# Kernel tuning notes

Hardware: AMD Instinct MI355X
Metric: run time of the kernel (lower is better)

The kernel has to match this reference:

```python
import jax, jax.numpy as jnp
import numpy as np

K = 100  # hard-coded in GWDLoss.forward


def _topk(scores, k=K):
    # CenterNet predict._topk: per-class topk then topk over classes.
    b, c, h, w = scores.shape
    topk_scores, topk_inds = jax.lax.top_k(scores.reshape(b, c, h * w), k)  # [b,c,k]
    topk_inds = topk_inds % (h * w)
    topk_ys = (topk_inds // w).astype(scores.dtype)
    topk_xs = (topk_inds % w).astype(scores.dtype)
    topk_score, topk_ind = jax.lax.top_k(topk_scores.reshape(b, c * k), k)  # [b,k]
    def g(t):
        return jnp.take_along_axis(t.reshape(b, c * k), topk_ind, axis=1)
    return topk_score, g(topk_inds), g(topk_xs), g(topk_ys)


def _transpose_and_gather_feat(feat, ind):
    b, c, h, w = feat.shape
    feat = feat.transpose(0, 2, 3, 1).reshape(b, h * w, c)  # [b,hw,c]
    idx = jnp.broadcast_to(ind[:, :, None], (b, ind.shape[1], c))
    return jnp.take_along_axis(feat, idx, axis=1)  # [b,K,c]


def xywhr2xyrs(xywhr):
    xywhr = xywhr.reshape(-1, 5)
    xy = xywhr[:, :2]
    wh = jnp.clip(xywhr[:, 2:4], 1e-7, 1e7)
    r = jnp.deg2rad(xywhr[:, 4])
    cos_r, sin_r = jnp.cos(r), jnp.sin(r)
    R = jnp.stack([cos_r, -sin_r, sin_r, cos_r], axis=-1).reshape(-1, 2, 2)
    S = 0.5 * wh[:, :, None] * jnp.eye(2, dtype=wh.dtype)  # diag_embed
    return xy, R, S


def gwd_loss(pred, target, tau=1.0, alpha=1.0):
    xy_p, R_p, S_p = xywhr2xyrs(pred)
    xy_t, R_t, S_t = xywhr2xyrs(target)
    xy_distance = jnp.sum((xy_p - xy_t) ** 2, axis=-1)
    Sigma_p = R_p @ (S_p ** 2) @ jnp.swapaxes(R_p, -1, -2)
    Sigma_t = R_t @ (S_t ** 2) @ jnp.swapaxes(R_t, -1, -2)
    dS_p = jnp.diagonal(S_p, axis1=-2, axis2=-1)
    dS_t = jnp.diagonal(S_t, axis1=-2, axis2=-1)
    whr = jnp.sum(dS_p ** 2, -1) + jnp.sum(dS_t ** 2, -1)
    _t = Sigma_p @ Sigma_t
    _t_tr = jnp.trace(_t, axis1=-2, axis2=-1)
    _t_det_sqrt = jnp.prod(dS_p, -1) * jnp.prod(dS_t, -1)
    whr = whr - 2.0 * jnp.sqrt(jnp.maximum(_t_tr + 2.0 * _t_det_sqrt, 0.0))
    distance = jnp.maximum(xy_distance + alpha * alpha * whr, 0.0)
    distance = jnp.log1p(distance)  # fun='log'
    return 1.0 - 1.0 / (tau + distance)  # tau=1.0 >= 1.0


def _forward(hm_p, ab_p, ang_p, hm_t, ab_t, ang_t, ind, reg_mask):
    mask = reg_mask.astype(jnp.float32)  # [B,K]
    pred_ab = _transpose_and_gather_feat(ab_p, ind)    # [B,K,2]
    pred_ang = _transpose_and_gather_feat(ang_p, ind)  # [B,K,1]
    mask_ab = mask[:, :, None]
    mask_ang = mask[:, :, None]
    _, _, xp, yp = _topk(hm_p)
    pred_xy = jnp.stack([xp, yp], axis=2)  # [B,K,2]
    pred = jnp.concatenate([pred_xy * mask_ab, pred_ab * 2.0 * mask_ab,
                            (pred_ang - 90.0) * mask_ang], axis=2)
    _, _, xt, yt = _topk(hm_t)
    target_xy = jnp.stack([xt, yt], axis=2)
    target = jnp.concatenate([target_xy * mask_ab, ab_t * 2.0 * mask_ab,
                              (ang_t - 90.0) * mask_ang], axis=2)
    return jnp.sum(gwd_loss(pred, target)) / (jnp.sum(mask) + 1e-8)


def setup_inputs() -> dict:
    key = jax.random.key(0)
    ks = jax.random.split(key, 8)
    B, H, W = 64, 256, 256
    return {
        "hm_p": jax.random.uniform(ks[0], (B, 1, H, W), jnp.float32),
        "ab_p": jax.random.uniform(ks[1], (B, 2, H, W), jnp.float32),
        "ang_p": jax.random.uniform(ks[2], (B, 1, H, W), jnp.float32),
        "hm_t": jax.random.uniform(ks[3], (B, 1, H, W), jnp.float32),
        "ab_t": jax.random.uniform(ks[4], (B, K, 2), jnp.float32),
        "ang_t": jax.random.uniform(ks[5], (B, K, 1), jnp.float32),
        "ind": jax.random.randint(ks[6], (B, K), 0, H * W, jnp.int32),
        "reg_mask": jax.random.randint(ks[7], (B, K), 0, 2, jnp.int32),
    }


def reference(hm_p, ab_p, ang_p, hm_t, ab_t, ang_t, ind, reg_mask):
    return _forward(hm_p, ab_p, ang_p, hm_t, ab_t, ang_t, ind, reg_mask)
```

## Files before the change

kernel.cpp:

```cpp
#include <hip/hip_runtime.h>
#include <stdint.h>

#define HW 65536
#define WIMG 256
#define TOPK 100
#define CAP2 2048
#define CAPC 64
#define NCHUNK 8
#define NGROUP 128
#define FTHR 512

__device__ __forceinline__ uint32_t fkey(float v) {
    uint32_t b = __float_as_uint(v);
    return b ^ ((b & 0x80000000u) ? 0xFFFFFFFFu : 0x80000000u);
}

#define CAND_OFF  0
#define CNT_OFF   524288
#define XY_OFF    528384
#define PART_OFF  630784
#define DONE_OFF  631296
#define WS_FAST_BYTES 631300

#define FILT_THR 0.9975f

#define AGENT __HIP_MEMORY_SCOPE_AGENT

__global__ __launch_bounds__(FTHR) void filter_kernel(
    const float* __restrict__ hm_p, const float* __restrict__ hm_t,
    unsigned long long* __restrict__ cand, uint32_t* __restrict__ chunkcnt)
{
    __shared__ unsigned long long lbuf[CAPC];
    __shared__ uint32_t lcnt;

    const int blk   = blockIdx.x;
    const int group = blk >> 3;
    const int chunk = blk & (NCHUNK - 1);
    const int which = group & 1;
    const int b     = group >> 1;
    const float* src = (which ? hm_t : hm_p) + (size_t)b * HW + chunk * (HW / NCHUNK);
    const float4* src4 = (const float4*)src;
    const int base0 = chunk * (HW / NCHUNK);

    if (threadIdx.x == 0) lcnt = 0;
    __syncthreads();

    #pragma unroll
    for (int t = 0; t < HW / NCHUNK / 4 / FTHR; ++t) {
        const int i = threadIdx.x + t * FTHR;
        float4 v = src4[i];
        const int base = base0 + i * 4;
        float f[4] = {v.x, v.y, v.z, v.w};
        #pragma unroll
        for (int e = 0; e < 4; ++e) {
            if (f[e] > FILT_THR) {
                uint32_t pos = atomicAdd(&lcnt, 1u);
                if (pos < CAPC)
                    lbuf[pos] = ((unsigned long long)fkey(f[e]) << 16) |
                                (unsigned long long)(65535 - (base + e));
            }
        }
    }
    __syncthreads();
    const uint32_t c = lcnt;
    if (threadIdx.x == 0) chunkcnt[blk] = c;
    unsigned long long* gc = cand + (size_t)blk * CAPC;
    if (threadIdx.x < min(c, (uint32_t)CAPC))
        gc[threadIdx.x] = lbuf[threadIdx.x];
}

__global__ __launch_bounds__(256) void sort_emit_kernel(
    const float* __restrict__ hm_p, const float* __restrict__ hm_t,
    const unsigned long long* __restrict__ cand, const uint32_t* __restrict__ chunkcnt,
    float* __restrict__ xy, uint32_t* __restrict__ done_cnt)
{
    __shared__ unsigned long long s[CAP2];
    __shared__ uint32_t s_cs[NCHUNK], s_off[NCHUNK];
    __shared__ uint32_t s_meta[2];
    __shared__ uint32_t s_cnt, s_kthr, s_klo, s_khi;

    const int tid   = threadIdx.x;
    const int group = blockIdx.x;
    const int which = group & 1;
    const int b     = group >> 1;

    if (group == 0 && tid == 0) *done_cnt = 0;

    if (tid < NCHUNK) s_cs[tid] = chunkcnt[group * NCHUNK + tid];
    __syncthreads();
    if (tid == 0) {
        uint32_t off = 0; int ok = 1;
        #pragma unroll
        for (int k = 0; k < NCHUNK; ++k) {
            s_off[k] = off;
            if (s_cs[k] > CAPC) ok = 0;
            off += s_cs[k];
        }
        s_meta[0] = off;
        s_meta[1] = (ok && off >= TOPK && off <= CAP2) ? 1u : 0u;
    }
    __syncthreads();

    uint32_t c;
    if (s_meta[1]) {
        const int k  = tid >> 5;
        const int i0 = tid & 31;
        const unsigned long long* gc = cand + (size_t)(group * NCHUNK + k) * CAPC;
        const uint32_t ck = s_cs[k], ofk = s_off[k];
        for (uint32_t i = i0; i < ck; i += 32) s[ofk + i] = gc[i];
        c = s_meta[0];
    } else {
        const float* src = (which ? hm_t : hm_p) + (size_t)b * HW;
        const float4* src4 = (const float4*)src;
        if (tid == 0) { s_kthr = fkey(0.99f); s_klo = 0u; s_khi = 0xFFFFFFFFu; }
        __syncthreads();
        for (int it = 0; it < 48; ++it) {
            if (tid == 0) s_cnt = 0;
            __syncthreads();
            const uint32_t kthr = s_kthr;
            for (int t = 0; t < HW / 4 / 256; ++t) {
                float4 v = src4[tid + t * 256];
                const int base = (tid + t * 256) * 4;
                float f[4] = {v.x, v.y, v.z, v.w};
                #pragma unroll
                for (int e = 0; e < 4; ++e) {
                    uint32_t uk = fkey(f[e]);
                    if (uk > kthr) {
                        uint32_t pos = atomicAdd(&s_cnt, 1u);
                        if (pos < CAP2)
                            s[pos] = ((unsigned long long)uk << 16) |
                                     (unsigned long long)(65535 - (base + e));
                    }
                }
            }
            __syncthreads();
            const uint32_t cc = s_cnt;
            if (cc >= TOPK && cc <= CAP2) break;
            if (tid == 0) {
                if (cc < TOPK) { s_khi = s_kthr; s_kthr = s_klo + ((s_kthr - s_klo) >> 1); }
                else           { s_klo = s_kthr; s_kthr = s_kthr + ((s_khi - s_kthr) >> 1); }
            }
            __syncthreads();
        }
        c = min(s_cnt, (uint32_t)CAP2);
    }
    __syncthreads();

    const int obase = which * 6400 + b * TOPK;

    if (c < TOPK) {
        for (int j = tid; j < TOPK; j += 256) {
            xy[obase + j]         = 255.f;
            xy[12800 + obase + j] = 255.f;
        }
        __syncthreads();
    }

    for (int i = tid; i < (int)c; i += 256) {
        const unsigned long long mine = s[i];
        int rank = 0;
        for (int j = 0; j < (int)c; ++j)
            rank += (s[j] > mine) ? 1 : 0;
        if (rank < TOPK) {
            uint32_t idx = 65535u - (uint32_t)(mine & 0xFFFFull);
            xy[obase + rank]         = (float)(idx & (WIMG - 1));
            xy[12800 + obase + rank] = (float)(idx >> 8);
        }
    }
}

__device__ __forceinline__ float gwd(float px, float py, float pw, float ph, float pr,
                                     float tx, float ty, float tw, float th, float trg)
{
    pw = fminf(fmaxf(pw, 1e-7f), 1e7f);  ph = fminf(fmaxf(ph, 1e-7f), 1e7f);
    tw = fminf(fmaxf(tw, 1e-7f), 1e7f);  th = fminf(fmaxf(th, 1e-7f), 1e7f);
    const float d2r = 0.017453292519943295f;
    float rp = pr * d2r, rt = trg * d2r;
    float cp = cosf(rp), sp = sinf(rp);
    float ct = cosf(rt), st = sinf(rt);
    float ap = 0.5f * pw, bp = 0.5f * ph;
    float at = 0.5f * tw, bt = 0.5f * th;
    float ap2 = ap * ap, bp2 = bp * bp, at2 = at * at, bt2 = bt * bt;
    float p00 = ap2 * cp * cp + bp2 * sp * sp;
    float p11 = ap2 * sp * sp + bp2 * cp * cp;
    float p01 = (ap2 - bp2) * cp * sp;
    float t00 = at2 * ct * ct + bt2 * st * st;
    float t11 = at2 * st * st + bt2 * ct * ct;
    float t01 = (at2 - bt2) * ct * st;
    float dx = px - tx, dy = py - ty;
    float xyd = dx * dx + dy * dy;
    float whr = ap2 + bp2 + at2 + bt2;
    float trc = p00 * t00 + 2.f * p01 * t01 + p11 * t11;
    float dets = (ap * bp) * (at * bt);
    whr -= 2.f * sqrtf(fmaxf(trc + 2.f * dets, 0.f));
    float dist = fmaxf(xyd + whr, 0.f);
    float d = log1pf(dist);
    return 1.f - 1.f / (1.f + d);
}

__global__ __launch_bounds__(128) void loss_final_kernel(
    const float* __restrict__ ab_p,  const float* __restrict__ ang_p,
    const float* __restrict__ ab_t,  const float* __restrict__ ang_t,
    const int*   __restrict__ ind,   const int*   __restrict__ reg_mask,
    const float* __restrict__ xy,    float* __restrict__ partials,
    uint32_t* __restrict__ done_cnt, float* __restrict__ out)
{
    const int b = blockIdx.x;
    const int j = threadIdx.x;
    float loss = 0.f, msum = 0.f;
    if (j < TOPK) {
        const int i = b * TOPK + j;
        float m = (float)reg_mask[i];
        msum = m;
        int id = ind[i];
        float xp = xy[i];
        float xt = xy[6400 + i];
        float yp = xy[12800 + i];
        float yt = xy[19200 + i];
        float ab0 = ab_p[(size_t)(b * 2 + 0) * HW + id];
        float ab1 = ab_p[(size_t)(b * 2 + 1) * HW + id];
        float ang = ang_p[(size_t)b * HW + id];
        float px = xp * m, py = yp * m;
        float pw = 2.f * ab0 * m, ph = 2.f * ab1 * m;
        float pr = (ang - 90.f) * m;
        float tx = xt * m, ty = yt * m;
        float tw = 2.f * ab_t[b * 200 + j * 2 + 0] * m;
        float th = 2.f * ab_t[b * 200 + j * 2 + 1] * m;
        float trg = (ang_t[i] - 90.f) * m;
        loss = gwd(px, py, pw, ph, pr, tx, ty, tw, th, trg);
    }
    #pragma unroll
    for (int off = 32; off > 0; off >>= 1) {
        loss += __shfl_down(loss, off);
        msum += __shfl_down(msum, off);
    }
    __shared__ float sl[2], sm[2];
    __shared__ uint32_t s_old;
    if ((threadIdx.x & 63) == 0) { sl[threadIdx.x >> 6] = loss; sm[threadIdx.x >> 6] = msum; }
    __syncthreads();
    if (threadIdx.x == 0) {
        __hip_atomic_store(&partials[b * 2],     sl[0] + sl[1], __ATOMIC_RELEASE, AGENT);
        __hip_atomic_store(&partials[b * 2 + 1], sm[0] + sm[1], __ATOMIC_RELEASE, AGENT);
        s_old = __hip_atomic_fetch_add(done_cnt, 1u, __ATOMIC_ACQ_REL, AGENT);
    }
    __syncthreads();
    if (s_old == 63u && threadIdx.x < 64) {
        float L = __hip_atomic_load(&partials[2 * threadIdx.x],     __ATOMIC_ACQUIRE, AGENT);
        float M = __hip_atomic_load(&partials[2 * threadIdx.x + 1], __ATOMIC_ACQUIRE, AGENT);
        #pragma unroll
        for (int off = 32; off > 0; off >>= 1) {
            L += __shfl_down(L, off);
            M += __shfl_down(M, off);
        }
        if (threadIdx.x == 0) out[0] = L / (M + 1e-8f);
    }
}

#define XY_OFF2    0
#define PART_OFF2  102400
#define FDONE_OFF2 102912

__global__ __launch_bounds__(1024) void topk_sort_kernel(
    const float* __restrict__ hm_p, const float* __restrict__ hm_t,
    float* __restrict__ xy, uint32_t* __restrict__ fdone)
{
    __shared__ unsigned long long s[CAP2];
    __shared__ uint32_t lcnt, s_kthr, s_klo, s_khi;

    const int tid   = threadIdx.x;
    const int group = blockIdx.x;
    const int which = group & 1;
    const int b     = group >> 1;

    if (group == 0 && tid == 0) *fdone = 0u;

    const float* src = (which ? hm_t : hm_p) + (size_t)b * HW;
    const float4* src4 = (const float4*)src;

    if (tid == 0) lcnt = 0;
    __syncthreads();
    #pragma unroll 4
    for (int t = 0; t < HW / 4 / 1024; ++t) {
        const int i = tid + t * 1024;
        float4 v = src4[i];
        const int base = i * 4;
        float f[4] = {v.x, v.y, v.z, v.w};
        #pragma unroll
        for (int e = 0; e < 4; ++e) {
            if (f[e] > FILT_THR) {
                uint32_t pos = atomicAdd(&lcnt, 1u);
                if (pos < CAP2)
                    s[pos] = ((unsigned long long)fkey(f[e]) << 16) |
                             (unsigned long long)(65535 - (base + e));
            }
        }
    }
    __syncthreads();
    uint32_t c = lcnt;

    if (c < TOPK || c > CAP2) {
        if (tid == 0) { s_kthr = fkey(0.99f); s_klo = 0u; s_khi = 0xFFFFFFFFu; }
        __syncthreads();
        for (int it = 0; it < 48; ++it) {
            if (tid == 0) lcnt = 0;
            __syncthreads();
            const uint32_t kthr = s_kthr;
            for (int t = 0; t < HW / 4 / 1024; ++t) {
                float4 v = src4[tid + t * 1024];
                const int base = (tid + t * 1024) * 4;
                float f[4] = {v.x, v.y, v.z, v.w};
                #pragma unroll
                for (int e = 0; e < 4; ++e) {
                    uint32_t uk = fkey(f[e]);
                    if (uk > kthr) {
                        uint32_t pos = atomicAdd(&lcnt, 1u);
                        if (pos < CAP2)
                            s[pos] = ((unsigned long long)uk << 16) |
                                     (unsigned long long)(65535 - (base + e));
                    }
                }
            }
            __syncthreads();
            const uint32_t cc = lcnt;
            if (cc >= TOPK && cc <= CAP2) break;
            if (tid == 0) {
                if (cc < TOPK) { s_khi = s_kthr; s_kthr = s_klo + ((s_kthr - s_klo) >> 1); }
                else           { s_klo = s_kthr; s_kthr = s_kthr + ((s_khi - s_kthr) >> 1); }
            }
            __syncthreads();
        }
        c = min(lcnt, (uint32_t)CAP2);
        __syncthreads();
    }

    int M = 128;
    while (M < (int)c) M <<= 1;
    for (int i = tid; i < M; i += 1024) if (i >= (int)c) s[i] = 0ull;
    __syncthreads();
    for (int len = 2; len <= M; len <<= 1) {
        for (int inc = len >> 1; inc > 0; inc >>= 1) {
            for (int i = tid; i < M; i += 1024) {
                int j = i ^ inc;
                if (j > i) {
                    bool desc = ((i & len) == 0);
                    unsigned long long a = s[i], d = s[j];
                    if ((a < d) == desc) { s[i] = d; s[j] = a; }
                }
            }
            __syncthreads();
        }
    }
    const int obase = which * 6400 + b * TOPK;
    for (int j = tid; j < TOPK; j += 1024) {
        unsigned long long key = s[j];
        uint32_t idx = 65535u - (uint32_t)(key & 0xFFFFull);
        xy[obase + j]         = (float)(idx & (WIMG - 1));
        xy[12800 + obase + j] = (float)(idx >> 8);
    }
}

extern "C" void kernel_launch(void* const* d_in, const int* in_sizes, int n_in,
                              void* d_out, int out_size, void* d_ws, size_t ws_size,
                              hipStream_t stream)
{
    const float* hm_p  = (const float*)d_in[0];
    const float* ab_p  = (const float*)d_in[1];
    const float* ang_p = (const float*)d_in[2];
    const float* hm_t  = (const float*)d_in[3];
    const float* ab_t  = (const float*)d_in[4];
    const float* ang_t = (const float*)d_in[5];
    const int*   ind      = (const int*)d_in[6];
    const int*   reg_mask = (const int*)d_in[7];
    float* out = (float*)d_out;

    if (ws_size >= WS_FAST_BYTES) {
        unsigned long long* cand = (unsigned long long*)((char*)d_ws + CAND_OFF);
        uint32_t* cnt   = (uint32_t*)((char*)d_ws + CNT_OFF);
        float*    xy    = (float*)((char*)d_ws + XY_OFF);
        float*    part  = (float*)((char*)d_ws + PART_OFF);
        uint32_t* done  = (uint32_t*)((char*)d_ws + DONE_OFF);

        filter_kernel<<<NGROUP * NCHUNK, FTHR, 0, stream>>>(hm_p, hm_t, cand, cnt);
        sort_emit_kernel<<<NGROUP, 256, 0, stream>>>(hm_p, hm_t, cand, cnt, xy, done);
        loss_final_kernel<<<64, 128, 0, stream>>>(ab_p, ang_p, ab_t, ang_t, ind,
                                                  reg_mask, xy, part, done, out);
    } else {
        float*    xy    = (float*)((char*)d_ws + XY_OFF2);
        float*    part  = (float*)((char*)d_ws + PART_OFF2);
        uint32_t* fdone = (uint32_t*)((char*)d_ws + FDONE_OFF2);
        topk_sort_kernel<<<NGROUP, 1024, 0, stream>>>(hm_p, hm_t, xy, fdone);
        loss_final_kernel<<<64, 128, 0, stream>>>(ab_p, ang_p, ab_t, ang_t, ind,
                                                  reg_mask, xy, part, fdone, out);
    }
}
```

Baseline: 21.43 us.

## Fuse top-k rank-sort and loss into one per-batch kernel

Replaces the separate sort_emit and loss_final kernels with a single rank_loss_kernel that, per batch, loads both heatmaps' candidates, ranks them in shared memory, and computes the GWD loss directly from shared xy without a global round-trip. This removes one kernel launch and the xy workspace buffer, and the done counter is now reset in the filter kernel. The trade-off is half as many blocks (64 instead of 128) for the ranking stage, each doing two sequential rankings, and 32KB of shared memory per block.

```diff
diff --git a/kernel.cpp b/kernel.cpp
--- a/kernel.cpp
+++ b/kernel.cpp
@@ -17,10 +17,9 @@
 
 #define CAND_OFF  0
 #define CNT_OFF   524288
-#define XY_OFF    528384
-#define PART_OFF  630784
-#define DONE_OFF  631296
-#define WS_FAST_BYTES 631300
+#define PART_OFF  528384
+#define DONE_OFF  528896
+#define WS_FAST_BYTES 528900
 
 #define FILT_THR 0.9975f
 
@@ -28,7 +27,8 @@
 
 __global__ __launch_bounds__(FTHR) void filter_kernel(
     const float* __restrict__ hm_p, const float* __restrict__ hm_t,
-    unsigned long long* __restrict__ cand, uint32_t* __restrict__ chunkcnt)
+    unsigned long long* __restrict__ cand, uint32_t* __restrict__ chunkcnt,
+    uint32_t* __restrict__ done_cnt)
 {
     __shared__ unsigned long long lbuf[CAPC];
     __shared__ uint32_t lcnt;
@@ -41,6 +41,8 @@
     const float* src = (which ? hm_t : hm_p) + (size_t)b * HW + chunk * (HW / NCHUNK);
     const float4* src4 = (const float4*)src;
     const int base0 = chunk * (HW / NCHUNK);
+
+    if (blk == 0 && threadIdx.x == 0) *done_cnt = 0;
 
     if (threadIdx.x == 0) lcnt = 0;
     __syncthreads();
@@ -67,106 +69,6 @@
     unsigned long long* gc = cand + (size_t)blk * CAPC;
     if (threadIdx.x < min(c, (uint32_t)CAPC))
         gc[threadIdx.x] = lbuf[threadIdx.x];
-}
-
-__global__ __launch_bounds__(256) void sort_emit_kernel(
-    const float* __restrict__ hm_p, const float* __restrict__ hm_t,
-    const unsigned long long* __restrict__ cand, const uint32_t* __restrict__ chunkcnt,
-    float* __restrict__ xy, uint32_t* __restrict__ done_cnt)
-{
-    __shared__ unsigned long long s[CAP2];
-    __shared__ uint32_t s_cs[NCHUNK], s_off[NCHUNK];
-    __shared__ uint32_t s_meta[2];
-    __shared__ uint32_t s_cnt, s_kthr, s_klo, s_khi;
-
-    const int tid   = threadIdx.x;
-    const int group = blockIdx.x;
-    const int which = group & 1;
-    const int b     = group >> 1;
-
-    if (group == 0 && tid == 0) *done_cnt = 0;
-
-    if (tid < NCHUNK) s_cs[tid] = chunkcnt[group * NCHUNK + tid];
-    __syncthreads();
-    if (tid == 0) {
-        uint32_t off = 0; int ok = 1;
-        #pragma unroll
-        for (int k = 0; k < NCHUNK; ++k) {
-            s_off[k] = off;
-            if (s_cs[k] > CAPC) ok = 0;
-            off += s_cs[k];
-        }
-        s_meta[0] = off;
-        s_meta[1] = (ok && off >= TOPK && off <= CAP2) ? 1u : 0u;
-    }
-    __syncthreads();
-
-    uint32_t c;
-    if (s_meta[1]) {
-        const int k  = tid >> 5;
-        const int i0 = tid & 31;
-        const unsigned long long* gc = cand + (size_t)(group * NCHUNK + k) * CAPC;
-        const uint32_t ck = s_cs[k], ofk = s_off[k];
-        for (uint32_t i = i0; i < ck; i += 32) s[ofk + i] = gc[i];
-        c = s_meta[0];
-    } else {
-        const float* src = (which ? hm_t : hm_p) + (size_t)b * HW;
-        const float4* src4 = (const float4*)src;
-        if (tid == 0) { s_kthr = fkey(0.99f); s_klo = 0u; s_khi = 0xFFFFFFFFu; }
-        __syncthreads();
-        for (int it = 0; it < 48; ++it) {
-            if (tid == 0) s_cnt = 0;
-            __syncthreads();
-            const uint32_t kthr = s_kthr;
-            for (int t = 0; t < HW / 4 / 256; ++t) {
-                float4 v = src4[tid + t * 256];
-                const int base = (tid + t * 256) * 4;
-                float f[4] = {v.x, v.y, v.z, v.w};
-                #pragma unroll
-                for (int e = 0; e < 4; ++e) {
-                    uint32_t uk = fkey(f[e]);
-                    if (uk > kthr) {
-                        uint32_t pos = atomicAdd(&s_cnt, 1u);
-                        if (pos < CAP2)
-                            s[pos] = ((unsigned long long)uk << 16) |
-                                     (unsigned long long)(65535 - (base + e));
-                    }
-                }
-            }
-            __syncthreads();
-            const uint32_t cc = s_cnt;
-            if (cc >= TOPK && cc <= CAP2) break;
-            if (tid == 0) {
-                if (cc < TOPK) { s_khi = s_kthr; s_kthr = s_klo + ((s_kthr - s_klo) >> 1); }
-                else           { s_klo = s_kthr; s_kthr = s_kthr + ((s_khi - s_kthr) >> 1); }
-            }
-            __syncthreads();
-        }
-        c = min(s_cnt, (uint32_t)CAP2);
-    }
-    __syncthreads();
-
-    const int obase = which * 6400 + b * TOPK;
-
-    if (c < TOPK) {
-        for (int j = tid; j < TOPK; j += 256) {
-            xy[obase + j]         = 255.f;
-            xy[12800 + obase + j] = 255.f;
-        }
-        __syncthreads();
-    }
-
-    for (int i = tid; i < (int)c; i += 256) {
-        const unsigned long long mine = s[i];
-        int rank = 0;
-        for (int j = 0; j < (int)c; ++j)
-            rank += (s[j] > mine) ? 1 : 0;
-        if (rank < TOPK) {
-            uint32_t idx = 65535u - (uint32_t)(mine & 0xFFFFull);
-            xy[obase + rank]         = (float)(idx & (WIMG - 1));
-            xy[12800 + obase + rank] = (float)(idx >> 8);
-        }
-    }
 }
 
 __device__ __forceinline__ float gwd(float px, float py, float pw, float ph, float pr,
@@ -198,6 +100,264 @@
     return 1.f - 1.f / (1.f + d);
 }
 
+__global__ __launch_bounds__(256) void rank_loss_kernel(
+    const float* __restrict__ hm_p, const float* __restrict__ hm_t,
+    const float* __restrict__ ab_p,  const float* __restrict__ ang_p,
+    const float* __restrict__ ab_t,  const float* __restrict__ ang_t,
+    const int*   __restrict__ ind,   const int*   __restrict__ reg_mask,
+    const unsigned long long* __restrict__ cand, const uint32_t* __restrict__ chunkcnt,
+    float* __restrict__ partials, uint32_t* __restrict__ done_cnt,
+    float* __restrict__ out)
+{
+    __shared__ unsigned long long s[2][CAP2];
+    __shared__ float xs[2][TOPK], ys[2][TOPK];
+    __shared__ uint32_t s_cs[2][NCHUNK], s_off[2][NCHUNK], s_tot[2], s_ok[2];
+    __shared__ uint32_t s_cnt, s_kthr, s_klo, s_khi, s_old;
+    __shared__ float sl[4], sm[4];
+
+    const int tid = threadIdx.x;
+    const int b   = blockIdx.x;
+
+    if (tid < 2 * NCHUNK) {
+        const int h = tid >> 3, k = tid & 7;
+        s_cs[h][k] = chunkcnt[(2 * b + h) * NCHUNK + k];
+    }
+    __syncthreads();
+    if (tid < 2) {
+        uint32_t off = 0; int ok = 1;
+        #pragma unroll
+        for (int k = 0; k < NCHUNK; ++k) {
+            s_off[tid][k] = off;
+            if (s_cs[tid][k] > CAPC) ok = 0;
+            off += s_cs[tid][k];
+        }
+        s_tot[tid] = off;
+        s_ok[tid]  = (ok && off >= TOPK && off <= CAP2) ? 1u : 0u;
+    }
+    if (tid < TOPK) {
+        xs[0][tid] = 255.f; ys[0][tid] = 255.f;
+        xs[1][tid] = 255.f; ys[1][tid] = 255.f;
+    }
+    __syncthreads();
+
+    for (int h = 0; h < 2; ++h) {
+        if (s_ok[h]) {
+            const int k  = tid >> 5;
+            const int i0 = tid & 31;
+            const unsigned long long* gc =
+                cand + (size_t)((2 * b + h) * NCHUNK + k) * CAPC;
+            const uint32_t ck = s_cs[h][k], ofk = s_off[h][k];
+            for (uint32_t i = i0; i < ck; i += 32) s[h][ofk + i] = gc[i];
+        }
+    }
+    __syncthreads();
+
+    for (int h = 0; h < 2; ++h) {
+        if (!s_ok[h]) {
+            const float* src = (h ? hm_t : hm_p) + (size_t)b * HW;
+            const float4* src4 = (const float4*)src;
+            if (tid == 0) { s_kthr = fkey(0.99f); s_klo = 0u; s_khi = 0xFFFFFFFFu; }
+            __syncthreads();
+            for (int it = 0; it < 48; ++it) {
+                if (tid == 0) s_cnt = 0;
+                __syncthreads();
+                const uint32_t kthr = s_kthr;
+                for (int t = 0; t < HW / 4 / 256; ++t) {
+                    float4 v = src4[tid + t * 256];
+                    const int base = (tid + t * 256) * 4;
+                    float f[4] = {v.x, v.y, v.z, v.w};
+                    #pragma unroll
+                    for (int e = 0; e < 4; ++e) {
+                        uint32_t uk = fkey(f[e]);
+                        if (uk > kthr) {
+                            uint32_t pos = atomicAdd(&s_cnt, 1u);
+                            if (pos < CAP2)
+                                s[h][pos] = ((unsigned long long)uk << 16) |
+                                            (unsigned long long)(65535 - (base + e));
+                        }
+                    }
+                }
+                __syncthreads();
+                const uint32_t cc = s_cnt;
+                if (cc >= TOPK && cc <= CAP2) break;
+                if (tid == 0) {
+                    if (cc < TOPK) { s_khi = s_kthr; s_kthr = s_klo + ((s_kthr - s_klo) >> 1); }
+                    else           { s_klo = s_kthr; s_kthr = s_kthr + ((s_khi - s_kthr) >> 1); }
+                }
+                __syncthreads();
+            }
+            if (tid == 0) s_tot[h] = min(s_cnt, (uint32_t)CAP2);
+            __syncthreads();
+        }
+    }
+    __syncthreads();
+
+    for (int h = 0; h < 2; ++h) {
+        const int c = (int)s_tot[h];
+        for (int i = tid; i < c; i += 256) {
+            const unsigned long long mine = s[h][i];
+            int rank = 0;
+            for (int j = 0; j < c; ++j)
+                rank += (s[h][j] > mine) ? 1 : 0;
+            if (rank < TOPK) {
+                uint32_t idx = 65535u - (uint32_t)(mine & 0xFFFFull);
+                xs[h][rank] = (float)(idx & (WIMG - 1));
+                ys[h][rank] = (float)(idx >> 8);
+            }
+        }
+    }
+    __syncthreads();
+
+    const int j = tid;
+    float loss = 0.f, msum = 0.f;
+    if (j < TOPK) {
+        const int i = b * TOPK + j;
+        float m = (float)reg_mask[i];
+        msum = m;
+        int id = ind[i];
+        float ab0 = ab_p[(size_t)(b * 2 + 0) * HW + id];
+        float ab1 = ab_p[(size_t)(b * 2 + 1) * HW + id];
+        float ang = ang_p[(size_t)b * HW + id];
+        float px = xs[0][j] * m, py = ys[0][j] * m;
+        float pw = 2.f * ab0 * m, ph = 2.f * ab1 * m;
+        float pr = (ang - 90.f) * m;
+        float tx = xs[1][j] * m, ty = ys[1][j] * m;
+        float tw = 2.f * ab_t[b * 200 + j * 2 + 0] * m;
+        float th = 2.f * ab_t[b * 200 + j * 2 + 1] * m;
+        float trg = (ang_t[i] - 90.f) * m;
+        loss = gwd(px, py, pw, ph, pr, tx, ty, tw, th, trg);
+    }
+    #pragma unroll
+    for (int off = 32; off > 0; off >>= 1) {
+        loss += __shfl_down(loss, off);
+        msum += __shfl_down(msum, off);
+    }
+    const int w = tid >> 6;
+    if ((tid & 63) == 0) { sl[w] = loss; sm[w] = msum; }
+    __syncthreads();
+    if (tid == 0) {
+        __hip_atomic_store(&partials[b * 2],     sl[0] + sl[1] + sl[2] + sl[3],
+                           __ATOMIC_RELEASE, AGENT);
+        __hip_atomic_store(&partials[b * 2 + 1], sm[0] + sm[1] + sm[2] + sm[3],
+                           __ATOMIC_RELEASE, AGENT);
+        s_old = __hip_atomic_fetch_add(done_cnt, 1u, __ATOMIC_ACQ_REL, AGENT);
+    }
+    __syncthreads();
+    if (s_old == 63u && tid < 64) {
+        float L = __hip_atomic_load(&partials[2 * tid],     __ATOMIC_ACQUIRE, AGENT);
+        float M = __hip_atomic_load(&partials[2 * tid + 1], __ATOMIC_ACQUIRE, AGENT);
+        #pragma unroll
+        for (int off = 32; off > 0; off >>= 1) {
+            L += __shfl_down(L, off);
+            M += __shfl_down(M, off);
+        }
+        if (tid == 0) out[0] = L / (M + 1e-8f);
+    }
+}
+
+#define XY_OFF2    0
+#define PART_OFF2  102400
+#define FDONE_OFF2 102912
+
+__global__ __launch_bounds__(1024) void topk_sort_kernel(
+    const float* __restrict__ hm_p, const float* __restrict__ hm_t,
+    float* __restrict__ xy, uint32_t* __restrict__ fdone)
+{
+    __shared__ unsigned long long s[CAP2];
+    __shared__ uint32_t lcnt, s_kthr, s_klo, s_khi;
+
+    const int tid   = threadIdx.x;
+    const int group = blockIdx.x;
+    const int which = group & 1;
+    const int b     = group >> 1;
+
+    if (group == 0 && tid == 0) *fdone = 0u;
+
+    const float* src = (which ? hm_t : hm_p) + (size_t)b * HW;
+    const float4* src4 = (const float4*)src;
+
+    if (tid == 0) lcnt = 0;
+    __syncthreads();
+    #pragma unroll 4
+    for (int t = 0; t < HW / 4 / 1024; ++t) {
+        const int i = tid + t * 1024;
+        float4 v = src4[i];
+        const int base = i * 4;
+        float f[4] = {v.x, v.y, v.z, v.w};
+        #pragma unroll
+        for (int e = 0; e < 4; ++e) {
+            if (f[e] > FILT_THR) {
+                uint32_t pos = atomicAdd(&lcnt, 1u);
+                if (pos < CAP2)
+                    s[pos] = ((unsigned long long)fkey(f[e]) << 16) |
+                             (unsigned long long)(65535 - (base + e));
+            }
+        }
+    }
+    __syncthreads();
+    uint32_t c = lcnt;
+
+    if (c < TOPK || c > CAP2) {
+        if (tid == 0) { s_kthr = fkey(0.99f); s_klo = 0u; s_khi = 0xFFFFFFFFu; }
+        __syncthreads();
+        for (int it = 0; it < 48; ++it) {
+            if (tid == 0) lcnt = 0;
+            __syncthreads();
+            const uint32_t kthr = s_kthr;
+            for (int t = 0; t < HW / 4 / 1024; ++t) {
+                float4 v = src4[tid + t * 1024];
+                const int base = (tid + t * 1024) * 4;
+                float f[4] = {v.x, v.y, v.z, v.w};
+                #pragma unroll
+                for (int e = 0; e < 4; ++e) {
+                    uint32_t uk = fkey(f[e]);
+                    if (uk > kthr) {
+                        uint32_t pos = atomicAdd(&lcnt, 1u);
+                        if (pos < CAP2)
+                            s[pos] = ((unsigned long long)uk << 16) |
+                                     (unsigned long long)(65535 - (base + e));
+                    }
+                }
+            }
+            __syncthreads();
+            const uint32_t cc = lcnt;
+            if (cc >= TOPK && cc <= CAP2) break;
+            if (tid == 0) {
+                if (cc < TOPK) { s_khi = s_kthr; s_kthr = s_klo + ((s_kthr - s_klo) >> 1); }
+                else           { s_klo = s_kthr; s_kthr = s_kthr + ((s_khi - s_kthr) >> 1); }
+            }
+            __syncthreads();
+        }
+        c = min(lcnt, (uint32_t)CAP2);
+        __syncthreads();
+    }
+
+    int M = 128;
+    while (M < (int)c) M <<= 1;
+    for (int i = tid; i < M; i += 1024) if (i >= (int)c) s[i] = 0ull;
+    __syncthreads();
+    for (int len = 2; len <= M; len <<= 1) {
+        for (int inc = len >> 1; inc > 0; inc >>= 1) {
+            for (int i = tid; i < M; i += 1024) {
+                int j = i ^ inc;
+                if (j > i) {
+                    bool desc = ((i & len) == 0);
+                    unsigned long long a = s[i], d = s[j];
+                    if ((a < d) == desc) { s[i] = d; s[j] = a; }
+                }
+            }
+            __syncthreads();
+        }
+    }
+    const int obase = which * 6400 + b * TOPK;
+    for (int j = tid; j < TOPK; j += 1024) {
+        unsigned long long key = s[j];
+        uint32_t idx = 65535u - (uint32_t)(key & 0xFFFFull);
+        xy[obase + j]         = (float)(idx & (WIMG - 1));
+        xy[12800 + obase + j] = (float)(idx >> 8);
+    }
+}
+
 __global__ __launch_bounds__(128) void loss_final_kernel(
     const float* __restrict__ ab_p,  const float* __restrict__ ang_p,
     const float* __restrict__ ab_t,  const float* __restrict__ ang_t,
@@ -256,109 +416,6 @@
     }
 }
 
-#define XY_OFF2    0
-#define PART_OFF2  102400
-#define FDONE_OFF2 102912
-
-__global__ __launch_bounds__(1024) void topk_sort_kernel(
-    const float* __restrict__ hm_p, const float* __restrict__ hm_t,
-    float* __restrict__ xy, uint32_t* __restrict__ fdone)
-{
-    __shared__ unsigned long long s[CAP2];
-    __shared__ uint32_t lcnt, s_kthr, s_klo, s_khi;
-
-    const int tid   = threadIdx.x;
-    const int group = blockIdx.x;
-    const int which = group & 1;
-    const int b     = group >> 1;
-
-    if (group == 0 && tid == 0) *fdone = 0u;
-
-    const float* src = (which ? hm_t : hm_p) + (size_t)b * HW;
-    const float4* src4 = (const float4*)src;
-
-    if (tid == 0) lcnt = 0;
-    __syncthreads();
-    #pragma unroll 4
-    for (int t = 0; t < HW / 4 / 1024; ++t) {
-        const int i = tid + t * 1024;
-        float4 v = src4[i];
-        const int base = i * 4;
-        float f[4] = {v.x, v.y, v.z, v.w};
-        #pragma unroll
-        for (int e = 0; e < 4; ++e) {
-            if (f[e] > FILT_THR) {
-                uint32_t pos = atomicAdd(&lcnt, 1u);
-                if (pos < CAP2)
-                    s[pos] = ((unsigned long long)fkey(f[e]) << 16) |
-                             (unsigned long long)(65535 - (base + e));
-            }
-        }
-    }
-    __syncthreads();
-    uint32_t c = lcnt;
-
-    if (c < TOPK || c > CAP2) {
-        if (tid == 0) { s_kthr = fkey(0.99f); s_klo = 0u; s_khi = 0xFFFFFFFFu; }
-        __syncthreads();
-        for (int it = 0; it < 48; ++it) {
-            if (tid == 0) lcnt = 0;
-            __syncthreads();
-            const uint32_t kthr = s_kthr;
-            for (int t = 0; t < HW / 4 / 1024; ++t) {
-                float4 v = src4[tid + t * 1024];
-                const int base = (tid + t * 1024) * 4;
-                float f[4] = {v.x, v.y, v.z, v.w};
-                #pragma unroll
-                for (int e = 0; e < 4; ++e) {
-                    uint32_t uk = fkey(f[e]);
-                    if (uk > kthr) {
-                        uint32_t pos = atomicAdd(&lcnt, 1u);
-                        if (pos < CAP2)
-                            s[pos] = ((unsigned long long)uk << 16) |
-                                     (unsigned long long)(65535 - (base + e));
-                    }
-                }
-            }
-            __syncthreads();
-            const uint32_t cc = lcnt;
-            if (cc >= TOPK && cc <= CAP2) break;
-            if (tid == 0) {
-                if (cc < TOPK) { s_khi = s_kthr; s_kthr = s_klo + ((s_kthr - s_klo) >> 1); }
-                else           { s_klo = s_kthr; s_kthr = s_kthr + ((s_khi - s_kthr) >> 1); }
-            }
-            __syncthreads();
-        }
-        c = min(lcnt, (uint32_t)CAP2);
-        __syncthreads();
-    }
-
-    int M = 128;
-    while (M < (int)c) M <<= 1;
-    for (int i = tid; i < M; i += 1024) if (i >= (int)c) s[i] = 0ull;
-    __syncthreads();
-    for (int len = 2; len <= M; len <<= 1) {
-        for (int inc = len >> 1; inc > 0; inc >>= 1) {
-            for (int i = tid; i < M; i += 1024) {
-                int j = i ^ inc;
-                if (j > i) {
-                    bool desc = ((i & len) == 0);
-                    unsigned long long a = s[i], d = s[j];
-                    if ((a < d) == desc) { s[i] = d; s[j] = a; }
-                }
-            }
-            __syncthreads();
-        }
-    }
-    const int obase = which * 6400 + b * TOPK;
-    for (int j = tid; j < TOPK; j += 1024) {
-        unsigned long long key = s[j];
-        uint32_t idx = 65535u - (uint32_t)(key & 0xFFFFull);
-        xy[obase + j]         = (float)(idx & (WIMG - 1));
-        xy[12800 + obase + j] = (float)(idx >> 8);
-    }
-}
-
 extern "C" void kernel_launch(void* const* d_in, const int* in_sizes, int n_in,
                               void* d_out, int out_size, void* d_ws, size_t ws_size,
                               hipStream_t stream)
@@ -376,14 +433,13 @@
     if (ws_size >= WS_FAST_BYTES) {
         unsigned long long* cand = (unsigned long long*)((char*)d_ws + CAND_OFF);
         uint32_t* cnt   = (uint32_t*)((char*)d_ws + CNT_OFF);
-        float*    xy    = (float*)((char*)d_ws + XY_OFF);
         float*    part  = (float*)((char*)d_ws + PART_OFF);
         uint32_t* done  = (uint32_t*)((char*)d_ws + DONE_OFF);
 
-        filter_kernel<<<NGROUP * NCHUNK, FTHR, 0, stream>>>(hm_p, hm_t, cand, cnt);
-        sort_emit_kernel<<<NGROUP, 256, 0, stream>>>(hm_p, hm_t, cand, cnt, xy, done);
-        loss_final_kernel<<<64, 128, 0, stream>>>(ab_p, ang_p, ab_t, ang_t, ind,
-                                                  reg_mask, xy, part, done, out);
+        filter_kernel<<<NGROUP * NCHUNK, FTHR, 0, stream>>>(hm_p, hm_t, cand, cnt, done);
+        rank_loss_kernel<<<64, 256, 0, stream>>>(
+            hm_p, hm_t, ab_p, ang_p, ab_t, ang_t, ind, reg_mask,
+            cand, cnt, part, done, out);
     } else {
         float*    xy    = (float*)((char*)d_ws + XY_OFF2);
         float*    part  = (float*)((char*)d_ws + PART_OFF2);
```

Result: slower. 22.42 us (+4.6%).

## Fuse top-k ranking and GWD loss into one kernel with atomic completion counters

Applied to the files above, without the earlier changes.

Merges the sort/emit kernel and the loss kernel into a single launch. For each batch, the second of the two blocks (pred and target heatmaps) to finish its ranking computes that batch's loss, and the last batch to finish does the final reduction. Counters are zeroed in the filter kernel. This removes one kernel launch and its inter-kernel gap, at the cost of agent-scope atomics and a serialized tail in the last finishing blocks.

```diff
diff --git a/kernel.cpp b/kernel.cpp
--- a/kernel.cpp
+++ b/kernel.cpp
@@ -19,8 +19,9 @@
 #define CNT_OFF   524288
 #define XY_OFF    528384
 #define PART_OFF  630784
-#define DONE_OFF  631296
-#define WS_FAST_BYTES 631300
+#define FDONE_OFF 631296
+#define BDONE_OFF 631300
+#define WS_FAST_BYTES 631556
 
 #define FILT_THR 0.9975f
 
@@ -28,7 +29,8 @@
 
 __global__ __launch_bounds__(FTHR) void filter_kernel(
     const float* __restrict__ hm_p, const float* __restrict__ hm_t,
-    unsigned long long* __restrict__ cand, uint32_t* __restrict__ chunkcnt)
+    unsigned long long* __restrict__ cand, uint32_t* __restrict__ chunkcnt,
+    uint32_t* __restrict__ fdone, uint32_t* __restrict__ bdone)
 {
     __shared__ unsigned long long lbuf[CAPC];
     __shared__ uint32_t lcnt;
@@ -42,6 +44,11 @@
     const float4* src4 = (const float4*)src;
     const int base0 = chunk * (HW / NCHUNK);
 
+    if (blk == 0) {
+        if (threadIdx.x < 64) bdone[threadIdx.x] = 0u;
+        if (threadIdx.x == 64) *fdone = 0u;
+    }
+
     if (threadIdx.x == 0) lcnt = 0;
     __syncthreads();
 
@@ -67,106 +74,6 @@
     unsigned long long* gc = cand + (size_t)blk * CAPC;
     if (threadIdx.x < min(c, (uint32_t)CAPC))
         gc[threadIdx.x] = lbuf[threadIdx.x];
-}
-
-__global__ __launch_bounds__(256) void sort_emit_kernel(
-    const float* __restrict__ hm_p, const float* __restrict__ hm_t,
-    const unsigned long long* __restrict__ cand, const uint32_t* __restrict__ chunkcnt,
-    float* __restrict__ xy, uint32_t* __restrict__ done_cnt)
-{
-    __shared__ unsigned long long s[CAP2];
-    __shared__ uint32_t s_cs[NCHUNK], s_off[NCHUNK];
-    __shared__ uint32_t s_meta[2];
-    __shared__ uint32_t s_cnt, s_kthr, s_klo, s_khi;
-
-    const int tid   = threadIdx.x;
-    const int group = blockIdx.x;
-    const int which = group & 1;
-    const int b     = group >> 1;
-
-    if (group == 0 && tid == 0) *done_cnt = 0;
-
-    if (tid < NCHUNK) s_cs[tid] = chunkcnt[group * NCHUNK + tid];
-    __syncthreads();
-    if (tid == 0) {
-        uint32_t off = 0; int ok = 1;
-        #pragma unroll
-        for (int k = 0; k < NCHUNK; ++k) {
-            s_off[k] = off;
-            if (s_cs[k] > CAPC) ok = 0;
-            off += s_cs[k];
-        }
-        s_meta[0] = off;
-        s_meta[1] = (ok && off >= TOPK && off <= CAP2) ? 1u : 0u;
-    }
-    __syncthreads();
-
-    uint32_t c;
-    if (s_meta[1]) {
-        const int k  = tid >> 5;
-        const int i0 = tid & 31;
-        const unsigned long long* gc = cand + (size_t)(group * NCHUNK + k) * CAPC;
-        const uint32_t ck = s_cs[k], ofk = s_off[k];
-        for (uint32_t i = i0; i < ck; i += 32) s[ofk + i] = gc[i];
-        c = s_meta[0];
-    } else {
-        const float* src = (which ? hm_t : hm_p) + (size_t)b * HW;
-        const float4* src4 = (const float4*)src;
-        if (tid == 0) { s_kthr = fkey(0.99f); s_klo = 0u; s_khi = 0xFFFFFFFFu; }
-        __syncthreads();
-        for (int it = 0; it < 48; ++it) {
-            if (tid == 0) s_cnt = 0;
-            __syncthreads();
-            const uint32_t kthr = s_kthr;
-            for (int t = 0; t < HW / 4 / 256; ++t) {
-                float4 v = src4[tid + t * 256];
-                const int base = (tid + t * 256) * 4;
-                float f[4] = {v.x, v.y, v.z, v.w};
-                #pragma unroll
-                for (int e = 0; e < 4; ++e) {
-                    uint32_t uk = fkey(f[e]);
-                    if (uk > kthr) {
-                        uint32_t pos = atomicAdd(&s_cnt, 1u);
-                        if (pos < CAP2)
-                            s[pos] = ((unsigned long long)uk << 16) |
-                                     (unsigned long long)(65535 - (base + e));
-                    }
-                }
-            }
-            __syncthreads();
-            const uint32_t cc = s_cnt;
-            if (cc >= TOPK && cc <= CAP2) break;
-            if (tid == 0) {
-                if (cc < TOPK) { s_khi = s_kthr; s_kthr = s_klo + ((s_kthr - s_klo) >> 1); }
-                else           { s_klo = s_kthr; s_kthr = s_kthr + ((s_khi - s_kthr) >> 1); }
-            }
-            __syncthreads();
-        }
-        c = min(s_cnt, (uint32_t)CAP2);
-    }
-    __syncthreads();
-
-    const int obase = which * 6400 + b * TOPK;
-
-    if (c < TOPK) {
-        for (int j = tid; j < TOPK; j += 256) {
-            xy[obase + j]         = 255.f;
-            xy[12800 + obase + j] = 255.f;
-        }
-        __syncthreads();
-    }
-
-    for (int i = tid; i < (int)c; i += 256) {
-        const unsigned long long mine = s[i];
-        int rank = 0;
-        for (int j = 0; j < (int)c; ++j)
-            rank += (s[j] > mine) ? 1 : 0;
-        if (rank < TOPK) {
-            uint32_t idx = 65535u - (uint32_t)(mine & 0xFFFFull);
-            xy[obase + rank]         = (float)(idx & (WIMG - 1));
-            xy[12800 + obase + rank] = (float)(idx >> 8);
-        }
-    }
 }
 
 __device__ __forceinline__ float gwd(float px, float py, float pw, float ph, float pr,
@@ -198,6 +105,273 @@
     return 1.f - 1.f / (1.f + d);
 }
 
+__global__ __launch_bounds__(256) void sort_loss_kernel(
+    const float* __restrict__ hm_p, const float* __restrict__ hm_t,
+    const float* __restrict__ ab_p,  const float* __restrict__ ang_p,
+    const float* __restrict__ ab_t,  const float* __restrict__ ang_t,
+    const int*   __restrict__ ind,   const int*   __restrict__ reg_mask,
+    const unsigned long long* __restrict__ cand, const uint32_t* __restrict__ chunkcnt,
+    float* __restrict__ xy, float* __restrict__ partials,
+    uint32_t* __restrict__ bdone, uint32_t* __restrict__ fdone,
+    float* __restrict__ out)
+{
+    __shared__ unsigned long long s[CAP2];
+    __shared__ uint32_t s_cs[NCHUNK], s_off[NCHUNK];
+    __shared__ uint32_t s_meta[2];
+    __shared__ uint32_t s_cnt, s_kthr, s_klo, s_khi, s_b, s_f;
+    __shared__ float sl[4], sm[4];
+
+    const int tid   = threadIdx.x;
+    const int group = blockIdx.x;
+    const int which = group & 1;
+    const int b     = group >> 1;
+
+    if (tid < NCHUNK) s_cs[tid] = chunkcnt[group * NCHUNK + tid];
+    __syncthreads();
+    if (tid == 0) {
+        uint32_t off = 0; int ok = 1;
+        #pragma unroll
+        for (int k = 0; k < NCHUNK; ++k) {
+            s_off[k] = off;
+            if (s_cs[k] > CAPC) ok = 0;
+            off += s_cs[k];
+        }
+        s_meta[0] = off;
+        s_meta[1] = (ok && off >= TOPK && off <= CAP2) ? 1u : 0u;
+    }
+    __syncthreads();
+
+    uint32_t c;
+    if (s_meta[1]) {
+        const int k  = tid >> 5;
+        const int i0 = tid & 31;
+        const unsigned long long* gc = cand + (size_t)(group * NCHUNK + k) * CAPC;
+        const uint32_t ck = s_cs[k], ofk = s_off[k];
+        for (uint32_t i = i0; i < ck; i += 32) s[ofk + i] = gc[i];
+        c = s_meta[0];
+    } else {
+        const float* src = (which ? hm_t : hm_p) + (size_t)b * HW;
+        const float4* src4 = (const float4*)src;
+        if (tid == 0) { s_kthr = fkey(0.99f); s_klo = 0u; s_khi = 0xFFFFFFFFu; }
+        __syncthreads();
+        for (int it = 0; it < 48; ++it) {
+            if (tid == 0) s_cnt = 0;
+            __syncthreads();
+            const uint32_t kthr = s_kthr;
+            for (int t = 0; t < HW / 4 / 256; ++t) {
+                float4 v = src4[tid + t * 256];
+                const int base = (tid + t * 256) * 4;
+                float f[4] = {v.x, v.y, v.z, v.w};
+                #pragma unroll
+                for (int e = 0; e < 4; ++e) {
+                    uint32_t uk = fkey(f[e]);
+                    if (uk > kthr) {
+                        uint32_t pos = atomicAdd(&s_cnt, 1u);
+                        if (pos < CAP2)
+                            s[pos] = ((unsigned long long)uk << 16) |
+                                     (unsigned long long)(65535 - (base + e));
+                    }
+                }
+            }
+            __syncthreads();
+            const uint32_t cc = s_cnt;
+            if (cc >= TOPK && cc <= CAP2) break;
+            if (tid == 0) {
+                if (cc < TOPK) { s_khi = s_kthr; s_kthr = s_klo + ((s_kthr - s_klo) >> 1); }
+                else           { s_klo = s_kthr; s_kthr = s_kthr + ((s_khi - s_kthr) >> 1); }
+            }
+            __syncthreads();
+        }
+        c = min(s_cnt, (uint32_t)CAP2);
+    }
+    __syncthreads();
+
+    const int obase = which * 6400 + b * TOPK;
+
+    if (c < TOPK) {
+        for (int j = tid; j < TOPK; j += 256) {
+            xy[obase + j]         = 255.f;
+            xy[12800 + obase + j] = 255.f;
+        }
+        __syncthreads();
+    }
+
+    for (int i = tid; i < (int)c; i += 256) {
+        const unsigned long long mine = s[i];
+        int rank = 0;
+        for (int j = 0; j < (int)c; ++j)
+            rank += (s[j] > mine) ? 1 : 0;
+        if (rank < TOPK) {
+            uint32_t idx = 65535u - (uint32_t)(mine & 0xFFFFull);
+            xy[obase + rank]         = (float)(idx & (WIMG - 1));
+            xy[12800 + obase + rank] = (float)(idx >> 8);
+        }
+    }
+
+    __syncthreads();
+    if (tid == 0)
+        s_b = __hip_atomic_fetch_add(&bdone[b], 1u, __ATOMIC_ACQ_REL, AGENT);
+    __syncthreads();
+    if (s_b != 1u) return;
+
+    {
+        const int j = tid;
+        float loss = 0.f, msum = 0.f;
+        if (j < TOPK) {
+            const int i = b * TOPK + j;
+            float m = (float)reg_mask[i];
+            msum = m;
+            int id = ind[i];
+            float xp = xy[i];
+            float xt = xy[6400 + i];
+            float yp = xy[12800 + i];
+            float yt = xy[19200 + i];
+            float ab0 = ab_p[(size_t)(b * 2 + 0) * HW + id];
+            float ab1 = ab_p[(size_t)(b * 2 + 1) * HW + id];
+            float ang = ang_p[(size_t)b * HW + id];
+            float px = xp * m, py = yp * m;
+            float pw = 2.f * ab0 * m, ph = 2.f * ab1 * m;
+            float pr = (ang - 90.f) * m;
+            float tx = xt * m, ty = yt * m;
+            float tw = 2.f * ab_t[b * 200 + j * 2 + 0] * m;
+            float th = 2.f * ab_t[b * 200 + j * 2 + 1] * m;
+            float trg = (ang_t[i] - 90.f) * m;
+            loss = gwd(px, py, pw, ph, pr, tx, ty, tw, th, trg);
+        }
+        #pragma unroll
+        for (int off = 32; off > 0; off >>= 1) {
+            loss += __shfl_down(loss, off);
+            msum += __shfl_down(msum, off);
+        }
+        const int w = tid >> 6;
+        if ((tid & 63) == 0) { sl[w] = loss; sm[w] = msum; }
+        __syncthreads();
+        if (tid == 0) {
+            __hip_atomic_store(&partials[b * 2],     sl[0] + sl[1] + sl[2] + sl[3],
+                               __ATOMIC_RELEASE, AGENT);
+            __hip_atomic_store(&partials[b * 2 + 1], sm[0] + sm[1] + sm[2] + sm[3],
+                               __ATOMIC_RELEASE, AGENT);
+            s_f = __hip_atomic_fetch_add(fdone, 1u, __ATOMIC_ACQ_REL, AGENT);
+        }
+        __syncthreads();
+        if (s_f != 63u) return;
+    }
+
+    if (tid < 64) {
+        float L = __hip_atomic_load(&partials[2 * tid],     __ATOMIC_ACQUIRE, AGENT);
+        float M = __hip_atomic_load(&partials[2 * tid + 1], __ATOMIC_ACQUIRE, AGENT);
+        #pragma unroll
+        for (int off = 32; off > 0; off >>= 1) {
+            L += __shfl_down(L, off);
+            M += __shfl_down(M, off);
+        }
+        if (tid == 0) out[0] = L / (M + 1e-8f);
+    }
+}
+
+#define XY_OFF2    0
+#define PART_OFF2  102400
+#define FDONE_OFF2 102912
+
+__global__ __launch_bounds__(1024) void topk_sort_kernel(
+    const float* __restrict__ hm_p, const float* __restrict__ hm_t,
+    float* __restrict__ xy, uint32_t* __restrict__ fdone)
+{
+    __shared__ unsigned long long s[CAP2];
+    __shared__ uint32_t lcnt, s_kthr, s_klo, s_khi;
+
+    const int tid   = threadIdx.x;
+    const int group = blockIdx.x;
+    const int which = group & 1;
+    const int b     = group >> 1;
+
+    if (group == 0 && tid == 0) *fdone = 0u;
+
+    const float* src = (which ? hm_t : hm_p) + (size_t)b * HW;
+    const float4* src4 = (const float4*)src;
+
+    if (tid == 0) lcnt = 0;
+    __syncthreads();
+    #pragma unroll 4
+    for (int t = 0; t < HW / 4 / 1024; ++t) {
+        const int i = tid + t * 1024;
+        float4 v = src4[i];
+        const int base = i * 4;
+        float f[4] = {v.x, v.y, v.z, v.w};
+        #pragma unroll
+        for (int e = 0; e < 4; ++e) {
+            if (f[e] > FILT_THR) {
+                uint32_t pos = atomicAdd(&lcnt, 1u);
+                if (pos < CAP2)
+                    s[pos] = ((unsigned long long)fkey(f[e]) << 16) |
+                             (unsigned long long)(65535 - (base + e));
+            }
+        }
+    }
+    __syncthreads();
+    uint32_t c = lcnt;
+
+    if (c < TOPK || c > CAP2) {
+        if (tid == 0) { s_kthr = fkey(0.99f); s_klo = 0u; s_khi = 0xFFFFFFFFu; }
+        __syncthreads();
+        for (int it = 0; it < 48; ++it) {
+            if (tid == 0) lcnt = 0;
+            __syncthreads();
+            const uint32_t kthr = s_kthr;
+            for (int t = 0; t < HW / 4 / 1024; ++t) {
+                float4 v = src4[tid + t * 1024];
+                const int base = (tid + t * 1024) * 4;
+                float f[4] = {v.x, v.y, v.z, v.w};
+                #pragma unroll
+                for (int e = 0; e < 4; ++e) {
+                    uint32_t uk = fkey(f[e]);
+                    if (uk > kthr) {
+                        uint32_t pos = atomicAdd(&lcnt, 1u);
+                        if (pos < CAP2)
+                            s[pos] = ((unsigned long long)uk << 16) |
+                                     (unsigned long long)(65535 - (base + e));
+                    }
+                }
+            }
+            __syncthreads();
+            const uint32_t cc = lcnt;
+            if (cc >= TOPK && cc <= CAP2) break;
+            if (tid == 0) {
+                if (cc < TOPK) { s_khi = s_kthr; s_kthr = s_klo + ((s_kthr - s_klo) >> 1); }
+                else           { s_klo = s_kthr; s_kthr = s_kthr + ((s_khi - s_kthr) >> 1); }
+            }
+            __syncthreads();
+        }
+        c = min(lcnt, (uint32_t)CAP2);
+        __syncthreads();
+    }
+
+    int M = 128;
+    while (M < (int)c) M <<= 1;
+    for (int i = tid; i < M; i += 1024) if (i >= (int)c) s[i] = 0ull;
+    __syncthreads();
+    for (int len = 2; len <= M; len <<= 1) {
+        for (int inc = len >> 1; inc > 0; inc >>= 1) {
+            for (int i = tid; i < M; i += 1024) {
+                int j = i ^ inc;
+                if (j > i) {
+                    bool desc = ((i & len) == 0);
+                    unsigned long long a = s[i], d = s[j];
+                    if ((a < d) == desc) { s[i] = d; s[j] = a; }
+                }
+            }
+            __syncthreads();
+        }
+    }
+    const int obase = which * 6400 + b * TOPK;
+    for (int j = tid; j < TOPK; j += 1024) {
+        unsigned long long key = s[j];
+        uint32_t idx = 65535u - (uint32_t)(key & 0xFFFFull);
+        xy[obase + j]         = (float)(idx & (WIMG - 1));
+        xy[12800 + obase + j] = (float)(idx >> 8);
+    }
+}
+
 __global__ __launch_bounds__(128) void loss_final_kernel(
     const float* __restrict__ ab_p,  const float* __restrict__ ang_p,
     const float* __restrict__ ab_t,  const float* __restrict__ ang_t,
@@ -256,109 +430,6 @@
     }
 }
 
-#define XY_OFF2    0
-#define PART_OFF2  102400
-#define FDONE_OFF2 102912
-
-__global__ __launch_bounds__(1024) void topk_sort_kernel(
-    const float* __restrict__ hm_p, const float* __restrict__ hm_t,
-    float* __restrict__ xy, uint32_t* __restrict__ fdone)
-{
-    __shared__ unsigned long long s[CAP2];
-    __shared__ uint32_t lcnt, s_kthr, s_klo, s_khi;
-
-    const int tid   = threadIdx.x;
-    const int group = blockIdx.x;
-    const int which = group & 1;
-    const int b     = group >> 1;
-
-    if (group == 0 && tid == 0) *fdone = 0u;
-
-    const float* src = (which ? hm_t : hm_p) + (size_t)b * HW;
-    const float4* src4 = (const float4*)src;
-
-    if (tid == 0) lcnt = 0;
-    __syncthreads();
-    #pragma unroll 4
-    for (int t = 0; t < HW / 4 / 1024; ++t) {
-        const int i = tid + t * 1024;
-        float4 v = src4[i];
-        const int base = i * 4;
-        float f[4] = {v.x, v.y, v.z, v.w};
-        #pragma unroll
-        for (int e = 0; e < 4; ++e) {
-            if (f[e] > FILT_THR) {
-                uint32_t pos = atomicAdd(&lcnt, 1u);
-                if (pos < CAP2)
-                    s[pos] = ((unsigned long long)fkey(f[e]) << 16) |
-                             (unsigned long long)(65535 - (base + e));
-            }
-        }
-    }
-    __syncthreads();
-    uint32_t c = lcnt;
-
-    if (c < TOPK || c > CAP2) {
-        if (tid == 0) { s_kthr = fkey(0.99f); s_klo = 0u; s_khi = 0xFFFFFFFFu; }
-        __syncthreads();
-        for (int it = 0; it < 48; ++it) {
-            if (tid == 0) lcnt = 0;
-            __syncthreads();
-            const uint32_t kthr = s_kthr;
-            for (int t = 0; t < HW / 4 / 1024; ++t) {
-                float4 v = src4[tid + t * 1024];
-                const int base = (tid + t * 1024) * 4;
-                float f[4] = {v.x, v.y, v.z, v.w};
-                #pragma unroll
-                for (int e = 0; e < 4; ++e) {
-                    uint32_t uk = fkey(f[e]);
-                    if (uk > kthr) {
-                        uint32_t pos = atomicAdd(&lcnt, 1u);
-                        if (pos < CAP2)
-                            s[pos] = ((unsigned long long)uk << 16) |
-                                     (unsigned long long)(65535 - (base + e));
-                    }
-                }
-            }
-            __syncthreads();
-            const uint32_t cc = lcnt;
-            if (cc >= TOPK && cc <= CAP2) break;
-            if (tid == 0) {
-                if (cc < TOPK) { s_khi = s_kthr; s_kthr = s_klo + ((s_kthr - s_klo) >> 1); }
-                else           { s_klo = s_kthr; s_kthr = s_kthr + ((s_khi - s_kthr) >> 1); }
-            }
-            __syncthreads();
-        }
-        c = min(lcnt, (uint32_t)CAP2);
-        __syncthreads();
-    }
-
-    int M = 128;
-    while (M < (int)c) M <<= 1;
-    for (int i = tid; i < M; i += 1024) if (i >= (int)c) s[i] = 0ull;
-    __syncthreads();
-    for (int len = 2; len <= M; len <<= 1) {
-        for (int inc = len >> 1; inc > 0; inc >>= 1) {
-            for (int i = tid; i < M; i += 1024) {
-                int j = i ^ inc;
-                if (j > i) {
-                    bool desc = ((i & len) == 0);
-                    unsigned long long a = s[i], d = s[j];
-                    if ((a < d) == desc) { s[i] = d; s[j] = a; }
-                }
-            }
-            __syncthreads();
-        }
-    }
-    const int obase = which * 6400 + b * TOPK;
-    for (int j = tid; j < TOPK; j += 1024) {
-        unsigned long long key = s[j];
-        uint32_t idx = 65535u - (uint32_t)(key & 0xFFFFull);
-        xy[obase + j]         = (float)(idx & (WIMG - 1));
-        xy[12800 + obase + j] = (float)(idx >> 8);
-    }
-}
-
 extern "C" void kernel_launch(void* const* d_in, const int* in_sizes, int n_in,
                               void* d_out, int out_size, void* d_ws, size_t ws_size,
                               hipStream_t stream)
@@ -378,12 +449,14 @@
         uint32_t* cnt   = (uint32_t*)((char*)d_ws + CNT_OFF);
         float*    xy    = (float*)((char*)d_ws + XY_OFF);
         float*    part  = (float*)((char*)d_ws + PART_OFF);
-        uint32_t* done  = (uint32_t*)((char*)d_ws + DONE_OFF);
-
-        filter_kernel<<<NGROUP * NCHUNK, FTHR, 0, stream>>>(hm_p, hm_t, cand, cnt);
-        sort_emit_kernel<<<NGROUP, 256, 0, stream>>>(hm_p, hm_t, cand, cnt, xy, done);
-        loss_final_kernel<<<64, 128, 0, stream>>>(ab_p, ang_p, ab_t, ang_t, ind,
-                                                  reg_mask, xy, part, done, out);
+        uint32_t* fdone = (uint32_t*)((char*)d_ws + FDONE_OFF);
+        uint32_t* bdone = (uint32_t*)((char*)d_ws + BDONE_OFF);
+
+        filter_kernel<<<NGROUP * NCHUNK, FTHR, 0, stream>>>(hm_p, hm_t, cand, cnt,
+                                                            fdone, bdone);
+        sort_loss_kernel<<<NGROUP, 256, 0, stream>>>(
+            hm_p, hm_t, ab_p, ang_p, ab_t, ang_t, ind, reg_mask,
+            cand, cnt, xy, part, bdone, fdone, out);
     } else {
         float*    xy    = (float*)((char*)d_ws + XY_OFF2);
         float*    part  = (float*)((char*)d_ws + PART_OFF2);
```

New measurement: 23.55 us. +9.9%, slower.
